# Kernel tuning notes

Measured on AMD Instinct MI355X. Metric: run time of the kernel, lower is better.

## Reference

```python
import jax, jax.numpy as jnp
import numpy as np

B, S, D = 2, 2048, 2048
H, HK = 16, 4          # n_heads, n_kv_heads
DK = D // H            # 128
REP = H // HK


def setup_inputs() -> dict:
    key = jax.random.key(0)
    ks = jax.random.split(key, 9)
    x = jax.random.normal(ks[0], (B, S, D), dtype=jnp.float32)
    # RoPE tables: [max_seq_len, d_k/2]
    inv_freq = 1.0 / (10000.0 ** (jnp.arange(0, DK, 2, dtype=jnp.float32) / DK))
    t = jnp.arange(S, dtype=jnp.float32)
    freqs = jnp.outer(t, inv_freq)  # [S, DK/2]
    freqs_cos = jnp.cos(freqs)
    freqs_sin = jnp.sin(freqs)
    sc = 0.02
    return {
        "x": x,
        "freqs_cos": freqs_cos,
        "freqs_sin": freqs_sin,
        "wq_w": jax.random.normal(ks[1], (D, D), dtype=jnp.float32) * sc,
        "wq_b": jnp.zeros((D,), dtype=jnp.float32),
        "wk_w": jax.random.normal(ks[2], (HK * DK, D), dtype=jnp.float32) * sc,
        "wk_b": jnp.zeros((HK * DK,), dtype=jnp.float32),
        "wv_w": jax.random.normal(ks[3], (HK * DK, D), dtype=jnp.float32) * sc,
        "wv_b": jnp.zeros((HK * DK,), dtype=jnp.float32),
        "wo_w": jax.random.normal(ks[4], (D, D), dtype=jnp.float32) * sc,
        "wo_b": jnp.zeros((D,), dtype=jnp.float32),
    }


def _apply_rope(t, cos, sin):
    # t: [b, h, s, dk]; cos/sin: [1, 1, s, dk/2]; interleaved pairs (even=real, odd=imag)
    tr = t[..., 0::2]
    ti = t[..., 1::2]
    out_r = tr * cos - ti * sin
    out_i = tr * sin + ti * cos
    return jnp.stack([out_r, out_i], axis=-1).reshape(t.shape)


def reference(x, freqs_cos, freqs_sin, wq_w, wq_b, wk_w, wk_b, wv_w, wv_b, wo_w, wo_b):
    b, s, d = x.shape
    q = (x @ wq_w.T + wq_b).reshape(b, s, H, DK).transpose(0, 2, 1, 3)   # [b,H,s,dk]
    k = (x @ wk_w.T + wk_b).reshape(b, s, HK, DK).transpose(0, 2, 1, 3)  # [b,HK,s,dk]
    v = (x @ wv_w.T + wv_b).reshape(b, s, HK, DK).transpose(0, 2, 1, 3)

    cos = freqs_cos[:s][None, None]  # [1,1,s,dk/2]
    sin = freqs_sin[:s][None, None]
    q = _apply_rope(q, cos, sin)
    k = _apply_rope(k, cos, sin)

    # GQA: group q heads by kv head instead of materializing repeat_kv
    qg = q.reshape(b, HK, REP, s, DK)
    scores = jnp.einsum("bgrqd,bgkd->bgrqk", qg, k) / jnp.sqrt(jnp.float32(DK))
    causal = jnp.triu(jnp.full((s, s), -jnp.inf, dtype=scores.dtype), k=1)
    attn = jax.nn.softmax(scores + causal, axis=-1)  # dropout=0.0 -> no-op
    out = jnp.einsum("bgrqk,bgkd->bgrqd", attn, v)   # [b,HK,REP,s,dk]
    out = out.reshape(b, H, s, DK).transpose(0, 2, 1, 3).reshape(b, s, d)
    return out @ wo_w.T + wo_b
```

## Files before the change

### kernel.cpp

```cpp
#include <hip/hip_runtime.h>

#define BDIM 2
#define SDIM 2048
#define DDIM 2048
#define HQ 16
#define HKV 4
#define DKH 128
#define NKV 512
#define NQKV 3072
#define MROWS 4096

typedef __attribute__((ext_vector_type(8))) short bf16x8;
typedef __attribute__((ext_vector_type(4))) float f32x4;
typedef __attribute__((ext_vector_type(8))) unsigned short u16x8;
typedef __attribute__((ext_vector_type(4))) unsigned short u16x4;

#define AS1 __attribute__((address_space(1)))
#define AS3 __attribute__((address_space(3)))

__device__ __forceinline__ unsigned short f2bf(float f) {
    union { float f; unsigned int u; } v; v.f = f;
    unsigned int r = v.u + 0x7FFFu + ((v.u >> 16) & 1u);
    return (unsigned short)(r >> 16);
}
__device__ __forceinline__ float bf2f(unsigned short u) {
    union { unsigned int u; float f; } v; v.u = ((unsigned int)u) << 16;
    return v.f;
}
__device__ __forceinline__ unsigned int pack2bf(float a, float b) {
    return (unsigned int)f2bf(a) | ((unsigned int)f2bf(b) << 16);
}

#define NX   ((size_t)MROWS * DDIM)
#define NWQ  ((size_t)DDIM * DDIM)
#define NWKV ((size_t)NKV * DDIM)
#define CAST_BLOCKS 18432
__global__ void cast_all(const float* __restrict__ x, const float* __restrict__ wq,
                         const float* __restrict__ wk, const float* __restrict__ wv,
                         const float* __restrict__ wo, unsigned short* __restrict__ dst,
                         const float* __restrict__ qb, const float* __restrict__ kb,
                         const float* __restrict__ vb, float* __restrict__ b3) {
    if (blockIdx.x >= CAST_BLOCKS) {
        int i = (blockIdx.x - CAST_BLOCKS) * 256 + threadIdx.x;
        if (i < DDIM) b3[i] = qb[i];
        else if (i < DDIM + NKV) b3[i] = kb[i - DDIM];
        else if (i < NQKV) b3[i] = vb[i - DDIM - NKV];
        return;
    }
    size_t i = ((size_t)blockIdx.x * blockDim.x + threadIdx.x) * 4;
    const size_t N0 = NX, N1 = N0 + NWQ, N2 = N1 + NWKV, N3 = N2 + NWKV;
    const float* src; size_t off;
    if (i < N0)      { src = x;  off = i; }
    else if (i < N1) { src = wq; off = i - N0; }
    else if (i < N2) { src = wk; off = i - N1; }
    else if (i < N3) { src = wv; off = i - N2; }
    else             { src = wo; off = i - N3; }
    float4 v = *(const float4*)(src + off);
    u16x4 o;
    o[0] = f2bf(v.x); o[1] = f2bf(v.y); o[2] = f2bf(v.z); o[3] = f2bf(v.w);
    *(u16x4*)(dst + i) = o;
}

__global__ void rope_trans(unsigned short* __restrict__ buf,
                           const float* __restrict__ cosT, const float* __restrict__ sinT,
                           unsigned short* __restrict__ Vt, float qscale) {
    if (blockIdx.x < MROWS) {
        int r = blockIdx.x, pos = r & (SDIM - 1);
        int col0 = threadIdx.x * 8;
        unsigned short* p = buf + (size_t)r * NQKV + col0;
        int i0 = (col0 & 127) >> 1;
        float4 c4 = *(const float4*)(cosT + pos * 64 + i0);
        float4 s4 = *(const float4*)(sinT + pos * 64 + i0);
        float sc = (col0 < DDIM) ? qscale : 1.f;
        u16x8 v = *(const u16x8*)p;
        u16x8 o;
        float cc[4] = {c4.x, c4.y, c4.z, c4.w}, ss[4] = {s4.x, s4.y, s4.z, s4.w};
#pragma unroll
        for (int k = 0; k < 4; ++k) {
            float xr = bf2f(v[2 * k]), xi = bf2f(v[2 * k + 1]);
            o[2 * k]     = f2bf((xr * cc[k] - xi * ss[k]) * sc);
            o[2 * k + 1] = f2bf((xr * ss[k] + xi * cc[k]) * sc);
        }
        *(u16x8*)p = o;
    } else {
        __shared__ unsigned short T[32][33];
        if (threadIdx.x >= 256) return;
        int t = blockIdx.x - MROWS;
        int s0 = (t & 63) * 32, d0 = ((t >> 6) & 15) * 32, b = t >> 10;
        int c = threadIdx.x & 31, r4 = threadIdx.x >> 5;
        for (int rr = r4; rr < 32; rr += 8)
            T[rr][c] = buf[(size_t)(b * SDIM + s0 + rr) * NQKV + (DDIM + NKV) + d0 + c];
        __syncthreads();
        int cp = ((c & 0x0C) << 1) | ((c & 0x10) >> 2) | (c & 3);
        for (int rr = r4; rr < 32; rr += 8)
            Vt[(size_t)(b * NKV + d0 + rr) * SDIM + s0 + cp] = T[c][rr];
    }
}

template <int BF16OUT>
__global__ __launch_bounds__(512, 2) void gemm8(
    const unsigned short* __restrict__ A,
    const unsigned short* __restrict__ Bm,
    const float* __restrict__ bias,
    void* __restrict__ Cv,
    int pitch, int Kdim) {
    __shared__ unsigned short As[2][2][8192];
    __shared__ unsigned short Bs[2][2][8192];

    const int tid = threadIdx.x;
    const int lane = tid & 63;
    const int wid = tid >> 6;
    const int ml = lane & 15, quad = lane >> 4;
    const int wm = wid >> 2, wn = wid & 3;
    const int bhf = wn >> 1;
    const int brb = (wn & 1) * 64;

    const int gx = gridDim.x;
    const int nwg = gx * gridDim.y;
    int w0 = blockIdx.y * gx + blockIdx.x;
    int wsw = (nwg & 7) ? w0 : ((w0 & 7) * (nwg >> 3) + (w0 >> 3));
    const int m0 = (wsw / gx) * 256, n0 = (wsw % gx) * 256;

    const int NT = Kdim >> 6;
    const int xr = ml & 7;

    const int sr = tid >> 3;
    const int sk = ((tid & 7) ^ (sr & 7)) * 8;
    const unsigned short* Ag0 = A + (size_t)(m0 + sr) * Kdim + sk;
    const unsigned short* Bg0 = Bm + (size_t)(n0 + sr) * Kdim + sk;
    const size_t rk64 = (size_t)64 * Kdim;

    f32x4 acc[8][4] = {};

#define STG_A(bf, hf, kt)                                                                       \
    do {                                                                                        \
        __builtin_amdgcn_global_load_lds(                                                       \
            (const AS1 unsigned int*)(Ag0 + (size_t)(hf) * 2 * rk64 + (kt)),                    \
            (AS3 unsigned int*)(&As[bf][hf][tid * 8]), 16, 0, 0);                               \
        __builtin_amdgcn_global_load_lds(                                                       \
            (const AS1 unsigned int*)(Ag0 + (size_t)(hf) * 2 * rk64 + rk64 + (kt)),             \
            (AS3 unsigned int*)(&As[bf][hf][4096 + tid * 8]), 16, 0, 0);                        \
    } while (0)
#define STG_B(bf, hf, kt)                                                                       \
    do {                                                                                        \
        __builtin_amdgcn_global_load_lds(                                                       \
            (const AS1 unsigned int*)(Bg0 + (size_t)(hf) * 2 * rk64 + (kt)),                    \
            (AS3 unsigned int*)(&Bs[bf][hf][tid * 8]), 16, 0, 0);                               \
        __builtin_amdgcn_global_load_lds(                                                       \
            (const AS1 unsigned int*)(Bg0 + (size_t)(hf) * 2 * rk64 + rk64 + (kt)),             \
            (AS3 unsigned int*)(&Bs[bf][hf][4096 + tid * 8]), 16, 0, 0);                        \
    } while (0)

    STG_B(0, 0, 0); STG_B(0, 1, 0);
    STG_A(0, 0, 0); STG_A(0, 1, 0);
    if (NT > 1) {
        STG_B(1, 0, 64); STG_B(1, 1, 64);
        asm volatile("s_waitcnt vmcnt(4)" ::: "memory");
    } else {
        asm volatile("s_waitcnt vmcnt(0)" ::: "memory");
    }
    __builtin_amdgcn_s_barrier();

    for (int G = 0; G < NT; ++G) {
        const int cur = G & 1, nxt = cur ^ 1;
        const int ktA = (G + 1) * 64, ktB = (G + 2) * 64;
        const unsigned short* Ah = As[cur][wm];
        const unsigned short* Bh = Bs[cur][bhf];

        bf16x8 bfr[4][2];
#pragma unroll
        for (int nj = 0; nj < 4; ++nj)
#pragma unroll
            for (int kk = 0; kk < 2; ++kk)
                bfr[nj][kk] = *(const bf16x8*)&Bh[(brb + nj * 16 + ml) * 64 + ((kk * 4 + quad) ^ xr) * 8];

#pragma unroll
        for (int p = 0; p < 4; ++p) {
            bf16x8 af[2][2];
#pragma unroll
            for (int mi = 0; mi < 2; ++mi)
#pragma unroll
                for (int kk = 0; kk < 2; ++kk)
                    af[mi][kk] = *(const bf16x8*)&Ah[((p * 2 + mi) * 16 + ml) * 64 + ((kk * 4 + quad) ^ xr) * 8];

            if (p == 0) {
                if (G + 1 < NT) { STG_A(nxt, 0, ktA); STG_A(nxt, 1, ktA); }
            } else if (p == 2) {
                if (G + 2 < NT) STG_B(cur, 0, ktB);
            } else if (p == 3) {
                if (G + 2 < NT) STG_B(cur, 1, ktB);
            }

            __builtin_amdgcn_s_barrier();
            __builtin_amdgcn_s_setprio(1);
#pragma unroll
            for (int kk = 0; kk < 2; ++kk)
#pragma unroll
                for (int mi = 0; mi < 2; ++mi)
#pragma unroll
                    for (int nj = 0; nj < 4; ++nj)
                        acc[p * 2 + mi][nj] = __builtin_amdgcn_mfma_f32_16x16x32_bf16(
                            af[mi][kk], bfr[nj][kk], acc[p * 2 + mi][nj], 0, 0, 0);
            __builtin_amdgcn_s_setprio(0);
            if (p == 3) {
                if (G < NT - 2)       { asm volatile("s_waitcnt vmcnt(4)" ::: "memory"); }
                else if (G == NT - 2) { asm volatile("s_waitcnt vmcnt(0)" ::: "memory"); }
            }
            __builtin_amdgcn_s_barrier();
        }
    }
#undef STG_A
#undef STG_B

#pragma unroll
    for (int nj = 0; nj < 4; ++nj) {
        const int col = n0 + wn * 64 + nj * 16 + ml;
        const float bj = bias[col];
#pragma unroll
        for (int mi = 0; mi < 8; ++mi) {
            const int row0 = m0 + wm * 128 + mi * 16 + quad * 4;
#pragma unroll
            for (int rr = 0; rr < 4; ++rr) {
                float v = acc[mi][nj][rr] + bj;
                if (BF16OUT)
                    ((unsigned short*)Cv)[(size_t)(row0 + rr) * pitch + col] = f2bf(v);
                else
                    ((float*)Cv)[(size_t)(row0 + rr) * pitch + col] = v;
            }
        }
    }
}

__global__ __launch_bounds__(256, 2) void attn_fwd(
    const unsigned short* __restrict__ Qp,
    const unsigned short* __restrict__ Kp,
    const unsigned short* __restrict__ Vt,
    unsigned short* __restrict__ O) {
    const int l = blockIdx.x;
    const int j = l & 15;
    const int h = (l >> 4) & 15;
    const int b = l >> 8;
    const int g = h >> 2;
    const int jh = 31 - j;
    const int tid = threadIdx.x;
    const int w = tid >> 6, lane = tid & 63;
    const int ml = lane & 15, quad = lane >> 4;
    const int rsub = lane >> 2, seg = lane & 3;
    const int pr = w >> 1;
    const int wsub = w & 1;

    __shared__ unsigned short Ks[2][4 * 64 * 32];
    __shared__ unsigned short Vs[2][2 * 128 * 32];

    int myqt = pr ? j : jh;
    int q0 = myqt * 64 + wsub * 32;

    bf16x8 aq[2][4];
    auto load_q = [&](int qt) {
#pragma unroll
        for (int g2 = 0; g2 < 2; ++g2) {
            const size_t qrow = (size_t)(b * SDIM + qt * 64 + wsub * 32 + g2 * 16 + ml);
#pragma unroll
            for (int kc = 0; kc < 4; ++kc)
                aq[g2][kc] = *(const bf16x8*)(Qp + qrow * NQKV + h * DKH + kc * 32 + quad * 8);
        }
    };
    load_q(myqt);

    f32x4 o_acc[2][8] = {};
    float l_acc[2] = {0.f, 0.f};

    auto store_out = [&](int qt) {
#pragma unroll
        for (int g2 = 0; g2 < 2; ++g2) {
            float lt = l_acc[g2];
            lt += __shfl_xor(lt, 16);
            lt += __shfl_xor(lt, 32);
            float inv = 1.f / lt;
            size_t rowbase = (size_t)(b * SDIM + qt * 64 + wsub * 32 + g2 * 16 + ml) * DDIM + h * DKH + quad * 4;
#pragma unroll
            for (int dt = 0; dt < 8; ++dt) {
                u16x4 ov;
#pragma unroll
                for (int r = 0; r < 4; ++r)
                    ov[r] = f2bf(o_acc[g2][dt][r] * inv);
                *(u16x4*)(O + rowbase + dt * 16) = ov;
            }
        }
    };

    for (int it = 0; it < 17; ++it) {
        int kt;
        if (pr == 0)       kt = it;
        else if (it <= j)  kt = it;
        else if (it <= 15) kt = 16 + it - j;
        else               kt = -1;

        __syncthreads();
        if (kt >= 0) {
            const int kb = kt * 64;
#pragma unroll
            for (int kc = 0; kc < 4; ++kc)
#pragma unroll
                for (int rh = 0; rh < 2; ++rh)
                    __builtin_amdgcn_global_load_lds(
                        (const AS1 unsigned int*)(Kp + (size_t)(b * SDIM + kb + rh * 32 + wsub * 16 + rsub) * NQKV + g * DKH + kc * 32 + seg * 8),
                        (AS3 unsigned int*)(&Ks[pr][kc * 2048 + rh * 1024 + wsub * 512 + lane * 8]), 16, 0, 0);
#pragma unroll
            for (int c = 0; c < 8; ++c) {
                int u = wsub * 8 + c, kc2 = u >> 3, rg = u & 7;
                __builtin_amdgcn_global_load_lds(
                    (const AS1 unsigned int*)(Vt + (size_t)(b * NKV + g * DKH + rg * 16 + rsub) * SDIM + kb + kc2 * 32 + seg * 8),
                    (AS3 unsigned int*)(&Vs[pr][u * 512 + lane * 8]), 16, 0, 0);
            }
        }
        __syncthreads();

        if (pr == 1 && it == j + 1) {
            store_out(j);
            myqt = jh; q0 = myqt * 64 + wsub * 32;
            load_q(jh);
#pragma unroll
            for (int g2 = 0; g2 < 2; ++g2) {
                l_acc[g2] = 0.f;
#pragma unroll
                for (int dt = 0; dt < 8; ++dt) o_acc[g2][dt] = (f32x4){0.f, 0.f, 0.f, 0.f};
            }
        }

        if (kt >= 0) {
            const int kb = kt * 64;
            __builtin_amdgcn_s_setprio(1);
            f32x4 st[2][4];
#pragma unroll
            for (int t = 0; t < 4; ++t) {
                bf16x8 ak[4];
#pragma unroll
                for (int kc = 0; kc < 4; ++kc)
                    ak[kc] = *(const bf16x8*)&Ks[pr][kc * 2048 + (t * 16 + ml) * 32 + quad * 8];
#pragma unroll
                for (int g2 = 0; g2 < 2; ++g2) {
                    f32x4 sc = {};
#pragma unroll
                    for (int kc = 0; kc < 4; ++kc)
                        sc = __builtin_amdgcn_mfma_f32_16x16x32_bf16(ak[kc], aq[g2][kc], sc, 0, 0, 0);
                    st[g2][t] = sc;
                }
            }

            if (kb + 63 > q0) {
#pragma unroll
                for (int g2 = 0; g2 < 2; ++g2) {
                    int qg = q0 + g2 * 16 + ml;
#pragma unroll
                    for (int t = 0; t < 4; ++t) {
                        int kvb = kb + t * 16 + quad * 4;
#pragma unroll
                        for (int r = 0; r < 4; ++r)
                            if (kvb + r > qg) st[g2][t][r] = -INFINITY;
                    }
                }
            }

            unsigned int pk[2][4][2];
#pragma unroll
            for (int g2 = 0; g2 < 2; ++g2) {
#pragma unroll
                for (int t = 0; t < 4; ++t) {
                    float p0 = __expf(st[g2][t][0] - 20.f);
                    float p1 = __expf(st[g2][t][1] - 20.f);
                    float p2 = __expf(st[g2][t][2] - 20.f);
                    float p3 = __expf(st[g2][t][3] - 20.f);
                    l_acc[g2] += (p0 + p1) + (p2 + p3);
                    pk[g2][t][0] = pack2bf(p0, p1);
                    pk[g2][t][1] = pack2bf(p2, p3);
                }
            }

#pragma unroll
            for (int c = 0; c < 2; ++c) {
                union { unsigned int u[4]; bf16x8 v; } pb[2];
#pragma unroll
                for (int g2 = 0; g2 < 2; ++g2) {
                    pb[g2].u[0] = pk[g2][2 * c][0];     pb[g2].u[1] = pk[g2][2 * c][1];
                    pb[g2].u[2] = pk[g2][2 * c + 1][0]; pb[g2].u[3] = pk[g2][2 * c + 1][1];
                }
#pragma unroll
                for (int dt = 0; dt < 8; ++dt) {
                    bf16x8 av = *(const bf16x8*)&Vs[pr][c * 4096 + (dt * 16 + ml) * 32 + quad * 8];
                    o_acc[0][dt] = __builtin_amdgcn_mfma_f32_16x16x32_bf16(av, pb[0].v, o_acc[0][dt], 0, 0, 0);
                    o_acc[1][dt] = __builtin_amdgcn_mfma_f32_16x16x32_bf16(av, pb[1].v, o_acc[1][dt], 0, 0, 0);
                }
            }
            __builtin_amdgcn_s_setprio(0);
        }
    }

    __syncthreads();
    float* Fo = (float*)&Ks[0][0];
    float* Fl = (float*)&Vs[0][0];
    if (pr == 0) {
#pragma unroll
        for (int g2 = 0; g2 < 2; ++g2) {
            Fl[(g2 * 2 + wsub) * 64 + lane] = l_acc[g2];
#pragma unroll
            for (int dt = 0; dt < 8; ++dt)
                *(f32x4*)&Fo[(g2 * 8 + dt) * 512 + wsub * 256 + lane * 4] = o_acc[g2][dt];
        }
    }
    __syncthreads();
    if (pr == 1) {
#pragma unroll
        for (int g2 = 0; g2 < 2; ++g2) {
            l_acc[g2] += Fl[(g2 * 2 + wsub) * 64 + lane];
#pragma unroll
            for (int dt = 0; dt < 8; ++dt) {
                f32x4 pa = *(const f32x4*)&Fo[(g2 * 8 + dt) * 512 + wsub * 256 + lane * 4];
#pragma unroll
                for (int r = 0; r < 4; ++r) o_acc[g2][dt][r] += pa[r];
            }
        }
        store_out(jh);
    }
}

extern "C" void kernel_launch(void* const* d_in, const int* in_sizes, int n_in,
                              void* d_out, int out_size, void* d_ws, size_t ws_size,
                              hipStream_t stream) {
    const float* x    = (const float*)d_in[0];
    const float* fcos = (const float*)d_in[1];
    const float* fsin = (const float*)d_in[2];
    const float* wq_w = (const float*)d_in[3];
    const float* wq_b = (const float*)d_in[4];
    const float* wk_w = (const float*)d_in[5];
    const float* wk_b = (const float*)d_in[6];
    const float* wv_w = (const float*)d_in[7];
    const float* wv_b = (const float*)d_in[8];
    const float* wo_w = (const float*)d_in[9];
    const float* wo_b = (const float*)d_in[10];
    float* out = (float*)d_out;

    char* ws = (char*)d_ws;
    size_t off = 0;
    auto alloc = [&](size_t bytes) {
        char* p = ws + off;
        off += (bytes + 255) & ~(size_t)255;
        return p;
    };
    unsigned short* xb  = (unsigned short*)alloc(NX * 2);
    unsigned short* W3  = (unsigned short*)alloc((size_t)NQKV * DDIM * 2);
    unsigned short* wob = (unsigned short*)alloc(NWQ * 2);
    float* b3           = (float*)alloc((size_t)NQKV * 4);
    unsigned short* qkv = (unsigned short*)alloc((size_t)MROWS * NQKV * 2);
    unsigned short* Vt  = (unsigned short*)alloc((size_t)BDIM * NKV * SDIM * 2);
    unsigned short* att = (unsigned short*)alloc((size_t)MROWS * DDIM * 2);

    cast_all<<<dim3(CAST_BLOCKS + 12), dim3(256), 0, stream>>>(
        x, wq_w, wk_w, wv_w, wo_w, xb, wq_b, wk_b, wv_b, b3);

    gemm8<1><<<dim3(NQKV / 256, MROWS / 256), 512, 0, stream>>>(xb, W3, b3, qkv, NQKV, DDIM);

    const float scale = 0.08838834764831845f;
    rope_trans<<<dim3(MROWS + 2048), dim3(320), 0, stream>>>(qkv, fcos, fsin, Vt, scale);

    attn_fwd<<<dim3(512), dim3(256), 0, stream>>>(qkv, qkv + DDIM, Vt, att);

    gemm8<0><<<dim3(DDIM / 256, MROWS / 256), 512, 0, stream>>>(att, wob, wo_b, out, DDIM, DDIM);
}
```

Before: 321.1 us.

## Restructure GEMM main loop into four quadrant phases with register-level fragment reuse

The GEMM inner loop is reorganized from four row-strip phases (all B fragments loaded up front) into four 64x32 quadrant phases. A and B fragments are reused across phases (A quadrant reused for two N halves, B halves reused for two M halves), and the global-to-LDS prefetches are interleaved per phase. Explicit lgkmcnt waits and sched_barriers pin the instruction schedule so MFMA blocks overlap with the next loads. This aims to cut register pressure and LDS read traffic per phase and improve overlap, at the cost of extra barriers per K-step.

Result: faster. 310.3 us (-3.3%).

```diff
diff --git a/kernel.cpp b/kernel.cpp
--- a/kernel.cpp
+++ b/kernel.cpp
@@ -98,7 +98,7 @@
 }
 
 template <int BF16OUT>
-__global__ __launch_bounds__(512, 2) void gemm8(
+__global__ __launch_bounds__(512, 2) void gemm256(
     const unsigned short* __restrict__ A,
     const unsigned short* __restrict__ Bm,
     const float* __restrict__ bias,
@@ -128,27 +128,55 @@
     const int sk = ((tid & 7) ^ (sr & 7)) * 8;
     const unsigned short* Ag0 = A + (size_t)(m0 + sr) * Kdim + sk;
     const unsigned short* Bg0 = Bm + (size_t)(n0 + sr) * Kdim + sk;
-    const size_t rk64 = (size_t)64 * Kdim;
 
     f32x4 acc[8][4] = {};
 
 #define STG_A(bf, hf, kt)                                                                       \
     do {                                                                                        \
-        __builtin_amdgcn_global_load_lds(                                                       \
-            (const AS1 unsigned int*)(Ag0 + (size_t)(hf) * 2 * rk64 + (kt)),                    \
-            (AS3 unsigned int*)(&As[bf][hf][tid * 8]), 16, 0, 0);                               \
-        __builtin_amdgcn_global_load_lds(                                                       \
-            (const AS1 unsigned int*)(Ag0 + (size_t)(hf) * 2 * rk64 + rk64 + (kt)),             \
-            (AS3 unsigned int*)(&As[bf][hf][4096 + tid * 8]), 16, 0, 0);                        \
+        _Pragma("unroll")                                                                       \
+        for (int ll = 0; ll < 2; ++ll)                                                          \
+            __builtin_amdgcn_global_load_lds(                                                   \
+                (const AS1 unsigned int*)(Ag0 + (size_t)((hf) * 128 + ll * 64) * Kdim + (kt)),  \
+                (AS3 unsigned int*)(&As[bf][hf][ll * 4096 + tid * 8]), 16, 0, 0);               \
     } while (0)
 #define STG_B(bf, hf, kt)                                                                       \
     do {                                                                                        \
-        __builtin_amdgcn_global_load_lds(                                                       \
-            (const AS1 unsigned int*)(Bg0 + (size_t)(hf) * 2 * rk64 + (kt)),                    \
-            (AS3 unsigned int*)(&Bs[bf][hf][tid * 8]), 16, 0, 0);                               \
-        __builtin_amdgcn_global_load_lds(                                                       \
-            (const AS1 unsigned int*)(Bg0 + (size_t)(hf) * 2 * rk64 + rk64 + (kt)),             \
-            (AS3 unsigned int*)(&Bs[bf][hf][4096 + tid * 8]), 16, 0, 0);                        \
+        _Pragma("unroll")                                                                       \
+        for (int ll = 0; ll < 2; ++ll)                                                          \
+            __builtin_amdgcn_global_load_lds(                                                   \
+                (const AS1 unsigned int*)(Bg0 + (size_t)((hf) * 128 + ll * 64) * Kdim + (kt)),  \
+                (AS3 unsigned int*)(&Bs[bf][hf][ll * 4096 + tid * 8]), 16, 0, 0);               \
+    } while (0)
+#define READ_A(dst, qm_)                                                                        \
+    do {                                                                                        \
+        _Pragma("unroll")                                                                       \
+        for (int f = 0; f < 4; ++f)                                                             \
+            _Pragma("unroll")                                                                   \
+            for (int kk = 0; kk < 2; ++kk)                                                      \
+                dst[f][kk] = *(const bf16x8*)&As[cur][wm][((qm_) * 64 + f * 16 + ml) * 64 +     \
+                                                         ((kk * 4 + quad) ^ xr) * 8];           \
+    } while (0)
+#define READ_B(dst, qn_)                                                                        \
+    do {                                                                                        \
+        _Pragma("unroll")                                                                       \
+        for (int f = 0; f < 2; ++f)                                                             \
+            _Pragma("unroll")                                                                   \
+            for (int kk = 0; kk < 2; ++kk)                                                      \
+                dst[f][kk] = *(const bf16x8*)&Bs[cur][bhf][(brb + (qn_) * 32 + f * 16 + ml) *   \
+                                                           64 + ((kk * 4 + quad) ^ xr) * 8];    \
+    } while (0)
+#define MM16(qm_, bq_, qn_)                                                                     \
+    do {                                                                                        \
+        _Pragma("unroll")                                                                       \
+        for (int kk = 0; kk < 2; ++kk)                                                          \
+            _Pragma("unroll")                                                                   \
+            for (int fm = 0; fm < 4; ++fm)                                                      \
+                _Pragma("unroll")                                                               \
+                for (int fn = 0; fn < 2; ++fn)                                                  \
+                    acc[(qm_) * 4 + fm][(qn_) * 2 + fn] =                                       \
+                        __builtin_amdgcn_mfma_f32_16x16x32_bf16(                                \
+                            af[fm][kk], bq_[fn][kk], acc[(qm_) * 4 + fm][(qn_) * 2 + fn],       \
+                            0, 0, 0);                                                           \
     } while (0)
 
     STG_B(0, 0, 0); STG_B(0, 1, 0);
@@ -160,68 +188,62 @@
         asm volatile("s_waitcnt vmcnt(0)" ::: "memory");
     }
     __builtin_amdgcn_s_barrier();
+    __builtin_amdgcn_sched_barrier(0);
 
     for (int G = 0; G < NT; ++G) {
         const int cur = G & 1, nxt = cur ^ 1;
         const int ktA = (G + 1) * 64, ktB = (G + 2) * 64;
-        const unsigned short* Ah = As[cur][wm];
-        const unsigned short* Bh = Bs[cur][bhf];
-
-        bf16x8 bfr[4][2];
-#pragma unroll
-        for (int nj = 0; nj < 4; ++nj)
-#pragma unroll
-            for (int kk = 0; kk < 2; ++kk)
-                bfr[nj][kk] = *(const bf16x8*)&Bh[(brb + nj * 16 + ml) * 64 + ((kk * 4 + quad) ^ xr) * 8];
-
-#pragma unroll
-        for (int p = 0; p < 4; ++p) {
-            bf16x8 af[2][2];
-#pragma unroll
-            for (int mi = 0; mi < 2; ++mi)
-#pragma unroll
-                for (int kk = 0; kk < 2; ++kk)
-                    af[mi][kk] = *(const bf16x8*)&Ah[((p * 2 + mi) * 16 + ml) * 64 + ((kk * 4 + quad) ^ xr) * 8];
-
-            if (p == 0) {
-                if (G + 1 < NT) { STG_A(nxt, 0, ktA); STG_A(nxt, 1, ktA); }
-            } else if (p == 2) {
-                if (G + 2 < NT) STG_B(cur, 0, ktB);
-            } else if (p == 3) {
-                if (G + 2 < NT) STG_B(cur, 1, ktB);
-            }
-
-            __builtin_amdgcn_s_barrier();
-            __builtin_amdgcn_s_setprio(1);
-#pragma unroll
-            for (int kk = 0; kk < 2; ++kk)
-#pragma unroll
-                for (int mi = 0; mi < 2; ++mi)
-#pragma unroll
-                    for (int nj = 0; nj < 4; ++nj)
-                        acc[p * 2 + mi][nj] = __builtin_amdgcn_mfma_f32_16x16x32_bf16(
-                            af[mi][kk], bfr[nj][kk], acc[p * 2 + mi][nj], 0, 0, 0);
-            __builtin_amdgcn_s_setprio(0);
-            if (p == 3) {
-                if (G < NT - 2)       { asm volatile("s_waitcnt vmcnt(4)" ::: "memory"); }
-                else if (G == NT - 2) { asm volatile("s_waitcnt vmcnt(0)" ::: "memory"); }
-            }
-            __builtin_amdgcn_s_barrier();
-        }
+        bf16x8 af[4][2], bq0[2][2], bq1[2][2];
+
+        READ_A(af, 0); READ_B(bq0, 0);
+        if (G + 1 < NT) STG_A(nxt, 0, ktA);
+        __builtin_amdgcn_s_barrier();
+        asm volatile("s_waitcnt lgkmcnt(0)" ::: "memory");
+        __builtin_amdgcn_sched_barrier(0);
+        __builtin_amdgcn_s_setprio(1); MM16(0, bq0, 0); __builtin_amdgcn_s_setprio(0);
+        __builtin_amdgcn_s_barrier();
+
+        READ_B(bq1, 1);
+        if (G + 1 < NT) STG_A(nxt, 1, ktA);
+        __builtin_amdgcn_s_barrier();
+        asm volatile("s_waitcnt lgkmcnt(0)" ::: "memory");
+        __builtin_amdgcn_sched_barrier(0);
+        __builtin_amdgcn_s_setprio(1); MM16(0, bq1, 1); __builtin_amdgcn_s_setprio(0);
+        __builtin_amdgcn_s_barrier();
+
+        READ_A(af, 1);
+        if (G + 2 < NT) STG_B(cur, 0, ktB);
+        __builtin_amdgcn_s_barrier();
+        asm volatile("s_waitcnt lgkmcnt(0)" ::: "memory");
+        __builtin_amdgcn_sched_barrier(0);
+        __builtin_amdgcn_s_setprio(1); MM16(1, bq0, 0); __builtin_amdgcn_s_setprio(0);
+        __builtin_amdgcn_s_barrier();
+
+        if (G + 2 < NT) STG_B(cur, 1, ktB);
+        __builtin_amdgcn_s_barrier();
+        __builtin_amdgcn_s_setprio(1); MM16(1, bq1, 1); __builtin_amdgcn_s_setprio(0);
+        if (G < NT - 2)       { asm volatile("s_waitcnt vmcnt(4)" ::: "memory"); }
+        else if (G == NT - 2) { asm volatile("s_waitcnt vmcnt(0)" ::: "memory"); }
+        __builtin_amdgcn_sched_barrier(0);
+        __builtin_amdgcn_s_barrier();
+        __builtin_amdgcn_sched_barrier(0);
     }
 #undef STG_A
 #undef STG_B
-
-#pragma unroll
-    for (int nj = 0; nj < 4; ++nj) {
-        const int col = n0 + wn * 64 + nj * 16 + ml;
+#undef READ_A
+#undef READ_B
+#undef MM16
+
+#pragma unroll
+    for (int nf = 0; nf < 4; ++nf) {
+        const int col = n0 + wn * 64 + nf * 16 + ml;
         const float bj = bias[col];
 #pragma unroll
-        for (int mi = 0; mi < 8; ++mi) {
-            const int row0 = m0 + wm * 128 + mi * 16 + quad * 4;
+        for (int mf = 0; mf < 8; ++mf) {
+            const int row0 = m0 + wm * 128 + mf * 16 + quad * 4;
 #pragma unroll
             for (int rr = 0; rr < 4; ++rr) {
-                float v = acc[mi][nj][rr] + bj;
+                float v = acc[mf][nf][rr] + bj;
                 if (BF16OUT)
                     ((unsigned short*)Cv)[(size_t)(row0 + rr) * pitch + col] = f2bf(v);
                 else
@@ -458,12 +480,14 @@
     cast_all<<<dim3(CAST_BLOCKS + 12), dim3(256), 0, stream>>>(
         x, wq_w, wk_w, wv_w, wo_w, xb, wq_b, wk_b, wv_b, b3);
 
-    gemm8<1><<<dim3(NQKV / 256, MROWS / 256), 512, 0, stream>>>(xb, W3, b3, qkv, NQKV, DDIM);
+    gemm256<1><<<dim3(NQKV / 256, MROWS / 256), 512, 0, stream>>>(
+        xb, W3, b3, qkv, NQKV, DDIM);
 
     const float scale = 0.08838834764831845f;
     rope_trans<<<dim3(MROWS + 2048), dim3(320), 0, stream>>>(qkv, fcos, fsin, Vt, scale);
 
     attn_fwd<<<dim3(512), dim3(256), 0, stream>>>(qkv, qkv + DDIM, Vt, att);
 
-    gemm8<0><<<dim3(DDIM / 256, MROWS / 256), 512, 0, stream>>>(att, wob, wo_b, out, DDIM, DDIM);
-}
+    gemm256<0><<<dim3(DDIM / 256, MROWS / 256), 512, 0, stream>>>(
+        att, wob, wo_b, out, DDIM, DDIM);
+}
```
